# Kernel tuning notes

Hardware: AMD Instinct MI355X
Metric: run time of the kernel (lower is better)

## Reference

```python
import jax, jax.numpy as jnp
import numpy as np

B, D, T, K = 8, 512, 2048, 8192


def setup_inputs() -> dict:
    key = jax.random.key(0)
    k1, k2 = jax.random.split(key)
    latents = jax.random.normal(k1, (B, D, T), dtype=jnp.float32)
    # nn.Embedding weight initialized uniform(-1/K, 1/K)
    embedding = jax.random.uniform(k2, (K, D), dtype=jnp.float32,
                                   minval=-1.0 / K, maxval=1.0 / K)
    return {"latents": latents, "embedding": embedding}


def reference(latents, embedding):
    # latents: [B, D, T] -> [B, T, D]
    x = jnp.transpose(latents, (0, 2, 1))
    # argmin over squared distance == argmin over cdist(p=2), so output matches torch.
    x_sq = jnp.sum(x * x, axis=-1, keepdims=True)            # [B, T, 1]
    e_sq = jnp.sum(embedding * embedding, axis=-1)           # [K]
    cross = jnp.einsum("btd,kd->btk", x, embedding)          # [B, T, K]
    dist2 = x_sq - 2.0 * cross + e_sq                        # [B, T, K]
    encoding_inds = jnp.argmin(dist2, axis=-1)               # [B, T] int
    quantized = embedding[encoding_inds]                     # [B, T, D]
    return jnp.transpose(quantized, (0, 2, 1))               # [B, D, T]
```

## Files before the change

### kernel.cpp

```cpp
#include <hip/hip_runtime.h>
#include <hip/hip_bf16.h>
#include <cstdint>

constexpr int Dv = 512;
constexpr int Tv = 2048;
constexpr int Kv = 8192;
constexpr int BT = 16384;

constexpr int BQ = 128;
constexpr int BK = 128;
constexpr int BD = 32;
constexpr int KSPL = 8;
constexpr int KPS = Kv / KSPL;

__global__ void vq_xsq(const float* __restrict__ lat, float* __restrict__ xsq) {
    int q = blockIdx.x * 256 + threadIdx.x;
    int b = q >> 11, t = q & 2047;
    const float* p = lat + (size_t)b * Dv * Tv + t;
    float a = 0.f;
    #pragma unroll 8
    for (int d = 0; d < Dv; ++d) {
        float v = p[(size_t)d * Tv];
        a = fmaf(v, v, a);
    }
    xsq[q] = a;
}

__global__ void vq_esq(const float* __restrict__ emb, float* __restrict__ esq) {
    int gid = blockIdx.x * 256 + threadIdx.x;
    int k = gid >> 6;
    int l = threadIdx.x & 63;
    const float* p = emb + (size_t)k * Dv + l;
    float a = 0.f;
    #pragma unroll
    for (int i = 0; i < 8; ++i) {
        float v = p[i * 64];
        a = fmaf(v, v, a);
    }
    #pragma unroll
    for (int off = 32; off; off >>= 1) a += __shfl_down(a, off, 64);
    if (l == 0) esq[k] = a;
}

__global__ void vq_init(unsigned long long* __restrict__ keys) {
    int q = blockIdx.x * 256 + threadIdx.x;
    keys[q] = 0xFFFFFFFFFFFFFFFFull;
}

__global__ __launch_bounds__(256, 4) void vq_main(
        const float* __restrict__ lat, const float* __restrict__ emb,
        const float* __restrict__ xsq, const float* __restrict__ esq,
        unsigned long long* __restrict__ keys) {
    __shared__ float Xs[BD][BQ];
    __shared__ float Es[BD][BK];

    const int tid = threadIdx.x;
    const int bid = blockIdx.x;
    const int qb = bid & 127;
    const int ks = bid >> 7;
    const int q0 = qb * BQ;
    const int b  = q0 >> 11;
    const int t0 = q0 & 2047;
    const int k0base = ks * KPS;

    const int tx = (tid & 7) | (((tid >> 6) & 1) << 3);
    const int ty = ((tid >> 3) & 7) | (((tid >> 7) & 1) << 3);

    const int sq   = tid & 31;
    const int srow = tid >> 5;
    const int dq   = tid & 7;
    const int ekk  = tid >> 3;
    const int fsw  = dq << 2;

    float best[8];
    int   bidx[8];
    float xs[8];
    #pragma unroll
    for (int i = 0; i < 8; ++i) {
        best[i] = 3.4e38f;
        bidx[i] = 0x7fffffff;
        xs[i] = xsq[q0 + ty * 8 + i];
    }

    const float* latb = lat + (size_t)b * Dv * Tv + t0;
    float* const esw = &Es[0][0];

    for (int kc = 0; kc < KPS / BK; ++kc) {
        const int k0 = k0base + kc * BK;
        float c[8][8];
        #pragma unroll
        for (int i = 0; i < 8; ++i)
            #pragma unroll
            for (int j = 0; j < 8; ++j) c[i][j] = 0.f;

        for (int dc = 0; dc < Dv / BD; ++dc) {
            const int d0 = dc * BD;
            __syncthreads();
            #pragma unroll
            for (int i = 0; i < 4; ++i) {
                int dd = srow + i * 8;
                float4 v = *(const float4*)(latb + (size_t)(d0 + dd) * Tv + sq * 4);
                *(float4*)&Xs[dd][sq * 4] = v;
            }
            #pragma unroll
            for (int i = 0; i < 4; ++i) {
                int kk = ekk + i * 32;
                float4 v = *(const float4*)(emb + (size_t)(k0 + kk) * Dv + d0 + dq * 4);
                int ksw = kk ^ fsw;
                esw[(dq * 4 + 0) * BK + ksw] = v.x;
                esw[(dq * 4 + 1) * BK + ksw] = v.y;
                esw[(dq * 4 + 2) * BK + ksw] = v.z;
                esw[(dq * 4 + 3) * BK + ksw] = v.w;
            }
            __syncthreads();

            #pragma unroll 4
            for (int dd = 0; dd < BD; ++dd) {
                const int g = (dd >> 2) << 2;
                const float4 xa = *(const float4*)&Xs[dd][ty * 8];
                const float4 xb = *(const float4*)&Xs[dd][ty * 8 + 4];
                const float4 ea = *(const float4*)&esw[dd * BK + ((tx * 8) ^ g)];
                const float4 eb = *(const float4*)&esw[dd * BK + ((tx * 8 + 4) ^ g)];
                #define VQ_ROW(i, XV)                       \
                    c[i][0] = fmaf(XV, ea.x, c[i][0]);      \
                    c[i][1] = fmaf(XV, ea.y, c[i][1]);      \
                    c[i][2] = fmaf(XV, ea.z, c[i][2]);      \
                    c[i][3] = fmaf(XV, ea.w, c[i][3]);      \
                    c[i][4] = fmaf(XV, eb.x, c[i][4]);      \
                    c[i][5] = fmaf(XV, eb.y, c[i][5]);      \
                    c[i][6] = fmaf(XV, eb.z, c[i][6]);      \
                    c[i][7] = fmaf(XV, eb.w, c[i][7]);
                VQ_ROW(0, xa.x) VQ_ROW(1, xa.y) VQ_ROW(2, xa.z) VQ_ROW(3, xa.w)
                VQ_ROW(4, xb.x) VQ_ROW(5, xb.y) VQ_ROW(6, xb.z) VQ_ROW(7, xb.w)
                #undef VQ_ROW
            }
        }

        float es8[8];
        #pragma unroll
        for (int j = 0; j < 8; ++j) es8[j] = esq[k0 + tx * 8 + j];
        #pragma unroll
        for (int i = 0; i < 8; ++i)
            #pragma unroll
            for (int j = 0; j < 8; ++j) {
                float dist = fmaf(-2.0f, c[i][j], xs[i]) + es8[j];
                int kk = k0 + tx * 8 + j;
                if (dist < best[i]) { best[i] = dist; bidx[i] = kk; }
            }
    }

    __syncthreads();
    float* redv = &Xs[0][0];
    int*   redi = (int*)&Es[0][0];
    #pragma unroll
    for (int i = 0; i < 8; ++i) {
        redv[(ty * 16 + tx) * 8 + i] = best[i];
        redi[(ty * 16 + tx) * 8 + i] = bidx[i];
    }
    __syncthreads();
    if (tid < 128) {
        int yy = tid >> 3, ii = tid & 7;
        float bv = 3.4e38f;
        int bi = 0x7fffffff;
        #pragma unroll
        for (int t = 0; t < 16; ++t) {
            float v = redv[(yy * 16 + t) * 8 + ii];
            int  ix = redi[(yy * 16 + t) * 8 + ii];
            if (v < bv || (v == bv && ix < bi)) { bv = v; bi = ix; }
        }
        int q = q0 + yy * 8 + ii;
        unsigned long long key =
            ((unsigned long long)__float_as_uint(bv) << 32) | (unsigned int)bi;
        atomicMin(&keys[q], key);
    }
}

__global__ void vq_gather(const float* __restrict__ emb,
                          const unsigned long long* __restrict__ keys,
                          float* __restrict__ out) {
    int blk = blockIdx.x;
    int tid = threadIdx.x;
    int tl = tid & 63, dg = tid >> 6;
    int q = blk * 64 + tl;
    int b = q >> 11, t = q & 2047;
    int idx = (int)(keys[q] & 0xFFFFFFFFull);
    const float* er = emb + (size_t)idx * Dv + dg * 128;
    float* ob = out + ((size_t)b * Dv + dg * 128) * Tv + t;
    #pragma unroll 8
    for (int i = 0; i < 128; ++i) ob[(size_t)i * Tv] = er[i];
}

extern "C" void kernel_launch(void* const* d_in, const int* in_sizes, int n_in,
                              void* d_out, int out_size, void* d_ws, size_t ws_size,
                              hipStream_t stream) {
    (void)in_sizes; (void)n_in; (void)out_size; (void)ws_size;
    const float* lat = (const float*)d_in[0];
    const float* emb = (const float*)d_in[1];
    float* out = (float*)d_out;

    char* ws = (char*)d_ws;
    float* xsq = (float*)(ws);
    float* esq = (float*)(ws + (64 << 10));
    unsigned long long* keys =
        (unsigned long long*)(ws + (96 << 10));

    vq_init <<<BT / 256, 256, 0, stream>>>(keys);
    vq_xsq  <<<BT / 256, 256, 0, stream>>>(lat, xsq);
    vq_esq  <<<Kv / 4,   256, 0, stream>>>(emb, esq);
    vq_main <<<(BT / BQ) * KSPL, 256, 0, stream>>>(lat, emb, xsq, esq, keys);
    vq_gather<<<BT / 64, 256, 0, stream>>>(emb, keys, out);
}
```

Before: 2.061 ms.

## Read latents directly from global memory and remap blocks to share query tiles

Drops the shared-memory staging tile for latents so each thread loads its eight query values per depth step straight from global memory, relying on cache for reuse across threads. Block indexing is reordered so consecutive blocks cover different codebook slices of the same query tile, improving cache locality of latent reads. This halves shared memory use and removes one staging copy. In exchange, global-load latency sits inside the inner FMA loop and many threads now issue redundant loads.

```diff
diff --git a/kernel.cpp b/kernel.cpp
--- a/kernel.cpp
+++ b/kernel.cpp
@@ -11,7 +11,7 @@
 constexpr int BK = 128;
 constexpr int BD = 32;
 constexpr int KSPL = 8;
-constexpr int KPS = Kv / KSPL;
+constexpr int NBLK = (BT / BQ) * KSPL;
 
 __global__ void vq_xsq(const float* __restrict__ lat, float* __restrict__ xsq) {
     int q = blockIdx.x * 256 + threadIdx.x;
@@ -51,23 +51,20 @@
         const float* __restrict__ lat, const float* __restrict__ emb,
         const float* __restrict__ xsq, const float* __restrict__ esq,
         unsigned long long* __restrict__ keys) {
-    __shared__ float Xs[BD][BQ];
     __shared__ float Es[BD][BK];
 
     const int tid = threadIdx.x;
     const int bid = blockIdx.x;
-    const int qb = bid & 127;
-    const int ks = bid >> 7;
+    const int qb  = bid >> 3;
+    const int sub = bid & 7;
     const int q0 = qb * BQ;
     const int b  = q0 >> 11;
     const int t0 = q0 & 2047;
-    const int k0base = ks * KPS;
+    const int kc0 = sub * 8;
 
     const int tx = (tid & 7) | (((tid >> 6) & 1) << 3);
     const int ty = ((tid >> 3) & 7) | (((tid >> 7) & 1) << 3);
 
-    const int sq   = tid & 31;
-    const int srow = tid >> 5;
     const int dq   = tid & 7;
     const int ekk  = tid >> 3;
     const int fsw  = dq << 2;
@@ -83,10 +80,11 @@
     }
 
     const float* latb = lat + (size_t)b * Dv * Tv + t0;
+    const float* latty = latb + ty * 8;
     float* const esw = &Es[0][0];
 
-    for (int kc = 0; kc < KPS / BK; ++kc) {
-        const int k0 = k0base + kc * BK;
+    for (int kc = kc0; kc < kc0 + 8; ++kc) {
+        const int k0 = kc * BK;
         float c[8][8];
         #pragma unroll
         for (int i = 0; i < 8; ++i)
@@ -96,12 +94,6 @@
         for (int dc = 0; dc < Dv / BD; ++dc) {
             const int d0 = dc * BD;
             __syncthreads();
-            #pragma unroll
-            for (int i = 0; i < 4; ++i) {
-                int dd = srow + i * 8;
-                float4 v = *(const float4*)(latb + (size_t)(d0 + dd) * Tv + sq * 4);
-                *(float4*)&Xs[dd][sq * 4] = v;
-            }
             #pragma unroll
             for (int i = 0; i < 4; ++i) {
                 int kk = ekk + i * 32;
@@ -117,8 +109,9 @@
             #pragma unroll 4
             for (int dd = 0; dd < BD; ++dd) {
                 const int g = (dd >> 2) << 2;
-                const float4 xa = *(const float4*)&Xs[dd][ty * 8];
-                const float4 xb = *(const float4*)&Xs[dd][ty * 8 + 4];
+                const float* xrow = latty + (size_t)(d0 + dd) * Tv;
+                const float4 xa = *(const float4*)(xrow);
+                const float4 xb = *(const float4*)(xrow + 4);
                 const float4 ea = *(const float4*)&esw[dd * BK + ((tx * 8) ^ g)];
                 const float4 eb = *(const float4*)&esw[dd * BK + ((tx * 8 + 4) ^ g)];
                 #define VQ_ROW(i, XV)                       \
@@ -150,8 +143,8 @@
     }
 
     __syncthreads();
-    float* redv = &Xs[0][0];
-    int*   redi = (int*)&Es[0][0];
+    float* redv = &Es[0][0];
+    int*   redi = (int*)&Es[16][0];
     #pragma unroll
     for (int i = 0; i < 8; ++i) {
         redv[(ty * 16 + tx) * 8 + i] = best[i];
@@ -207,6 +200,6 @@
     vq_init <<<BT / 256, 256, 0, stream>>>(keys);
     vq_xsq  <<<BT / 256, 256, 0, stream>>>(lat, xsq);
     vq_esq  <<<Kv / 4,   256, 0, stream>>>(emb, esq);
-    vq_main <<<(BT / BQ) * KSPL, 256, 0, stream>>>(lat, emb, xsq, esq, keys);
+    vq_main <<<NBLK, 256, 0, stream>>>(lat, emb, xsq, esq, keys);
     vq_gather<<<BT / 64, 256, 0, stream>>>(emb, keys, out);
 }
```

Measured after the change: 2.394 ms. 1.16x slower.
